# Performance work log

Hardware: AMD Instinct MI355X
Metric: run time of the kernel (lower is better)

Reference implementation:

```python
import jax, jax.numpy as jnp
import numpy as np

LN_EPS = 1e-5


def _ln(x, g, b):
    mu = jnp.mean(x, -1, keepdims=True)
    xc = x - mu
    inv = jax.lax.rsqrt(jnp.mean(xc * xc, -1, keepdims=True) + LN_EPS)
    return xc * inv * g + b


def _subm_conv(x, nbr, W, b):
    # Submanifold 3D conv via rulebook gather-GEMM-accumulate.
    # x: [N, Cin], nbr: [N, K] neighbor row ids (-1 = missing), W: [K, Cin, Cout], b: [Cout]
    N = x.shape[0]
    xp = jnp.concatenate([x, jnp.zeros((1, x.shape[1]), x.dtype)], 0)  # sentinel zero row
    idx = jnp.where(nbr < 0, N, nbr)  # missing neighbors -> zero row
    acc0 = jnp.zeros((N, W.shape[-1]), x.dtype) + b
    def body(acc, xs):
        i, Wk = xs  # i: [N], Wk: [Cin, Cout]
        return acc + xp[i] @ Wk, None
    acc, _ = jax.lax.scan(body, acc0, (idx.T, W))
    return acc


def _blk1(x, W, b, g, be):  # 1x1x1 SubMConv + LN + ReLU
    return jax.nn.relu(_ln(x @ W + b, g, be))


def _blk3(x, nbr, W, b, g, be):  # 3x3x3 SubMConv + LN + ReLU
    return jax.nn.relu(_ln(_subm_conv(x, nbr, W, b), g, be))


def setup_inputs() -> dict:
    rng = np.random.default_rng(0)
    B, D, Npb, K = 2, 160, 131072, 27
    dim, half = 64, 32
    # Build random sparse voxel set and the rulebook (neighbor table) like spconv does.
    lookup = np.full((B, D, D, D), -1, np.int64)
    coords = np.zeros((B * Npb, 3), np.int64)
    for b in range(B):
        lin = np.sort(rng.choice(D * D * D, size=Npb, replace=False))
        z, y, x = np.unravel_index(lin, (D, D, D))
        rows = np.arange(b * Npb, (b + 1) * Npb)
        lookup[b, z, y, x] = rows
        coords[rows] = np.stack([z, y, x], 1)
    bidx = np.repeat(np.arange(B), Npb)
    offs = np.stack(np.meshgrid(np.arange(-1, 2), np.arange(-1, 2), np.arange(-1, 2), indexing="ij"), -1).reshape(K, 3)
    nz = coords[:, None, :] + offs[None]  # [N, K, 3]
    valid = ((nz >= 0) & (nz < D)).all(-1)
    nzc = np.clip(nz, 0, D - 1)
    nbr = lookup[bidx[:, None], nzc[..., 0], nzc[..., 1], nzc[..., 2]]
    nbr = np.where(valid, nbr, -1).astype(np.int32)

    key = jax.random.key(0)
    ks = iter(jax.random.split(key, 16))
    f32 = jnp.float32
    d = {"voxel_features": jax.random.normal(next(ks), (B * Npb, dim), f32),
         "nbr_idx": jnp.asarray(nbr)}
    def lnp(c):
        return jnp.ones((c,), f32), jnp.zeros((c,), f32)
    d["W1"] = 0.05 * jax.random.normal(next(ks), (dim, dim), f32); d["b1"] = jnp.zeros((dim,), f32); d["g1"], d["be1"] = lnp(dim)
    d["W2"] = 0.05 * jax.random.normal(next(ks), (dim, dim), f32); d["b2"] = jnp.zeros((dim,), f32); d["g2"], d["be2"] = lnp(dim)
    d["W3"] = 0.05 * jax.random.normal(next(ks), (K, dim, half), f32); d["b3"] = jnp.zeros((half,), f32); d["g3"], d["be3"] = lnp(half)
    d["W4"] = 0.05 * jax.random.normal(next(ks), (K, half, half), f32); d["b4"] = jnp.zeros((half,), f32); d["g4"], d["be4"] = lnp(half)
    d["W5"] = 0.05 * jax.random.normal(next(ks), (K, half, half), f32); d["b5"] = jnp.zeros((half,), f32); d["g5"], d["be5"] = lnp(half)
    d["W6"] = 0.05 * jax.random.normal(next(ks), (K, half, half), f32); d["b6"] = jnp.zeros((half,), f32); d["g6"], d["be6"] = lnp(half)
    d["W7"] = 0.05 * jax.random.normal(next(ks), (4 * dim, dim), f32); d["b7"] = jnp.zeros((dim,), f32); d["g7"], d["be7"] = lnp(dim)
    return d


def reference(voxel_features, nbr_idx,
              W1, b1, g1, be1, W2, b2, g2, be2,
              W3, b3, g3, be3, W4, b4, g4, be4,
              W5, b5, g5, be5, W6, b6, g6, be6,
              W7, b7, g7, be7):
    x = voxel_features
    f1 = _blk1(x, W1, b1, g1, be1)
    f2 = _blk1(x, W2, b2, g2, be2)
    feats = [f1, f2]
    f2 = _blk3(f2, nbr_idx, W3, b3, g3, be3); feats.append(f2)
    f2 = _blk3(f2, nbr_idx, W4, b4, g4, be4); feats.append(f2)
    f2 = _blk3(f2, nbr_idx, W5, b5, g5, be5); feats.append(f2)
    f2 = _blk3(f2, nbr_idx, W6, b6, g6, be6); feats.append(f2)
    cat = jnp.concatenate(feats, -1)  # [N, 4*dim]
    return _blk1(cat, W7, b7, g7, be7)
```

## Files before the change

kernel.cpp:

```cpp
#include <hip/hip_runtime.h>

typedef __attribute__((ext_vector_type(4))) float  float4_;
typedef __attribute__((ext_vector_type(8))) short  short8;
typedef __attribute__((ext_vector_type(8))) __bf16 bf16x8;

__device__ inline unsigned short f2bf(float f) {
    unsigned u = __builtin_bit_cast(unsigned, f);
    u += 0x7FFFu + ((u >> 16) & 1u);
    return (unsigned short)(u >> 16);
}

__device__ inline float4_ mfma16(bf16x8 a, bf16x8 b, float4_ c) {
    return __builtin_amdgcn_mfma_f32_16x16x32_bf16(a, b, c, 0, 0, 0);
}

__device__ inline void packW_one(const float* __restrict__ src, unsigned short* __restrict__ dst,
                                 int cin, int cout, int e) {
    int f = e >> 9, i = e & 511, lane = i >> 3, t = i & 7;
    int ntn = cout >> 4, ctn = cin >> 5;
    int nt = f % ntn;
    int rest = f / ntn;
    int ct = rest % ctn;
    int k = rest / ctn;
    int c = ct * 32 + (lane >> 4) * 8 + t;
    int j = nt * 16 + (lane & 15);
    dst[e] = f2bf(src[(k * cin + c) * cout + j]);
}

__global__ void pack_all_kernel(
    const float* __restrict__ W1, const float* __restrict__ W2,
    const float* __restrict__ W3, const float* __restrict__ W4,
    const float* __restrict__ W5, const float* __restrict__ W6,
    const float* __restrict__ W7,
    unsigned short* cat, unsigned short* Wp12, unsigned short* Wp3,
    unsigned short* Wp4, unsigned short* Wp5, unsigned short* Wp6,
    unsigned short* Wp7, int N) {
    int e = blockIdx.x * 256 + threadIdx.x;
    if (e < 8192) {
        int f = e >> 9, i = e & 511, lane = i >> 3, t = i & 7;
        int nt = f & 7, ct = f >> 3;
        int c = ct * 32 + (lane >> 4) * 8 + t;
        int j = nt * 16 + (lane & 15);
        float v = (j < 64) ? W1[c * 64 + j] : W2[c * 64 + (j - 64)];
        Wp12[e] = f2bf(v);
        return;
    }
    e -= 8192;
    if (e < 55296) { packW_one(W3, Wp3, 64, 32, e); return; }
    e -= 55296;
    if (e < 27648) { packW_one(W4, Wp4, 32, 32, e); return; }
    e -= 27648;
    if (e < 27648) { packW_one(W5, Wp5, 32, 32, e); return; }
    e -= 27648;
    if (e < 27648) { packW_one(W6, Wp6, 32, 32, e); return; }
    e -= 27648;
    if (e < 16384) { packW_one(W7, Wp7, 256, 64, e); return; }
    e -= 16384;
    if (e < 128) ((unsigned*)(cat + (size_t)N * 256))[e] = 0;
}

__global__ __launch_bounds__(256) void blk12_kernel(
    const float* __restrict__ x, unsigned short* cat,
    const unsigned short* __restrict__ Wp,
    const float* __restrict__ b1, const float* __restrict__ g1, const float* __restrict__ be1,
    const float* __restrict__ b2, const float* __restrict__ g2, const float* __restrict__ be2) {
    int tid = threadIdx.x, lane = tid & 63, wv = tid >> 6;
    int l15 = lane & 15, q = lane >> 4;
    long base = ((long)blockIdx.x * 4 + wv) * 16;

    float4_ acc[8];
#pragma unroll
    for (int i = 0; i < 8; i++) acc[i] = (float4_){0.f, 0.f, 0.f, 0.f};

#pragma unroll
    for (int kt = 0; kt < 2; kt++) {
        const float* xp = x + (base + l15) * 64 + kt * 32 + q * 8;
        float4_ f0 = *(const float4_*)xp;
        float4_ f1 = *(const float4_*)(xp + 4);
        short8 as;
        as[0] = (short)f2bf(f0[0]); as[1] = (short)f2bf(f0[1]);
        as[2] = (short)f2bf(f0[2]); as[3] = (short)f2bf(f0[3]);
        as[4] = (short)f2bf(f1[0]); as[5] = (short)f2bf(f1[1]);
        as[6] = (short)f2bf(f1[2]); as[7] = (short)f2bf(f1[3]);
        bf16x8 a = __builtin_bit_cast(bf16x8, as);
        const unsigned short* wp = Wp + (size_t)kt * 8 * 512;
#pragma unroll
        for (int nt = 0; nt < 8; nt++) {
            bf16x8 w = *(const bf16x8*)(wp + nt * 512 + lane * 8);
            acc[nt] = mfma16(a, w, acc[nt]);
        }
    }

    float bc[8], gc[8], bec[8];
#pragma unroll
    for (int nt = 0; nt < 8; nt++) {
        int j = nt * 16 + l15;
        if (j < 64) { bc[nt] = b1[j]; gc[nt] = g1[j]; bec[nt] = be1[j]; }
        else        { bc[nt] = b2[j - 64]; gc[nt] = g2[j - 64]; bec[nt] = be2[j - 64]; }
    }

#pragma unroll
    for (int r = 0; r < 4; r++) {
        long row = base + q * 4 + r;
        float v[8], s0 = 0.f, s1 = 0.f, q0 = 0.f, q1 = 0.f;
#pragma unroll
        for (int nt = 0; nt < 4; nt++) { v[nt] = acc[nt][r] + bc[nt]; s0 += v[nt]; q0 += v[nt] * v[nt]; }
#pragma unroll
        for (int nt = 4; nt < 8; nt++) { v[nt] = acc[nt][r] + bc[nt]; s1 += v[nt]; q1 += v[nt] * v[nt]; }
#pragma unroll
        for (int m = 1; m < 16; m <<= 1) {
            s0 += __shfl_xor(s0, m); q0 += __shfl_xor(q0, m);
            s1 += __shfl_xor(s1, m); q1 += __shfl_xor(q1, m);
        }
        float mu0 = s0 * (1.f / 64), var0 = q0 * (1.f / 64) - mu0 * mu0, inv0 = rsqrtf(var0 + 1e-5f);
        float mu1 = s1 * (1.f / 64), var1 = q1 * (1.f / 64) - mu1 * mu1, inv1 = rsqrtf(var1 + 1e-5f);
        unsigned short* cp = cat + row * 256;
#pragma unroll
        for (int nt = 0; nt < 4; nt++) {
            float y = fmaxf((v[nt] - mu0) * inv0 * gc[nt] + bec[nt], 0.f);
            cp[nt * 16 + l15] = f2bf(y);
        }
#pragma unroll
        for (int nt = 4; nt < 8; nt++) {
            float y = fmaxf((v[nt] - mu1) * inv1 * gc[nt] + bec[nt], 0.f);
            cp[nt * 16 + l15] = f2bf(y);
        }
    }
}

template <int CT, int D>
__global__ __launch_bounds__(256) void conv_kernel(
    unsigned short* cat, const int* __restrict__ nbr,
    const unsigned short* __restrict__ Wp,
    const float* __restrict__ bb, const float* __restrict__ gg, const float* __restrict__ bee,
    int in_off, int out_off, int N) {
    const int MT = 2;
    int tid = threadIdx.x, lane = tid & 63, wv = tid >> 6;
    int l15 = lane & 15, q = lane >> 4;
    int G = gridDim.x;
    int eff = (blockIdx.x & 7) * (G >> 3) + (blockIdx.x >> 3);
    long base = ((long)eff * 4 + wv) * 32;

    float4_ acc[MT][2];
#pragma unroll
    for (int mt = 0; mt < MT; mt++) {
        acc[mt][0] = (float4_){0.f, 0.f, 0.f, 0.f};
        acc[mt][1] = (float4_){0.f, 0.f, 0.f, 0.f};
    }

    const unsigned short* catp = cat + in_off + q * 8;
    const unsigned short* wl = Wp + lane * 8;
    const int* nbp[MT];
#pragma unroll
    for (int mt = 0; mt < MT; mt++) nbp[mt] = nbr + (base + mt * 16 + l15) * 27;

    bf16x8 f[D + 1][MT][CT];
    bf16x8 wr[3][CT][2];
    int rawi[3][MT];

    int raw0[D + 2][MT];
#pragma unroll
    for (int j = 0; j < D + 2; j++)
#pragma unroll
        for (int mt = 0; mt < MT; mt++) raw0[j][mt] = nbp[mt][j];

#pragma unroll
    for (int kk = 0; kk < 2; kk++)
#pragma unroll
        for (int ct = 0; ct < CT; ct++)
#pragma unroll
            for (int nt = 0; nt < 2; nt++)
                wr[kk][ct][nt] = *(const bf16x8*)(wl + ((size_t)((kk * CT + ct) * 2 + nt)) * 512);

#pragma unroll
    for (int j = 0; j < D; j++)
#pragma unroll
        for (int mt = 0; mt < MT; mt++) {
            int v = raw0[j][mt];
            size_t s = (size_t)(v < 0 ? N : v);
#pragma unroll
            for (int ct = 0; ct < CT; ct++)
                f[j][mt][ct] = *(const bf16x8*)(catp + s * 256 + ct * 32);
        }
#pragma unroll
    for (int mt = 0; mt < MT; mt++) {
        rawi[D % 3][mt] = raw0[D][mt];
        rawi[(D + 1) % 3][mt] = raw0[D + 1][mt];
    }

#pragma unroll
    for (int k = 0; k < 27; k++) {
        if (k + 2 < 27) {
#pragma unroll
            for (int ct = 0; ct < CT; ct++)
#pragma unroll
                for (int nt = 0; nt < 2; nt++)
                    wr[(k + 2) % 3][ct][nt] =
                        *(const bf16x8*)(wl + ((size_t)(((k + 2) * CT + ct) * 2 + nt)) * 512);
        }
        if (k + D < 27) {
#pragma unroll
            for (int mt = 0; mt < MT; mt++) {
                int v = rawi[(k + D) % 3][mt];
                size_t s = (size_t)(v < 0 ? N : v);
#pragma unroll
                for (int ct = 0; ct < CT; ct++)
                    f[(k + D) % (D + 1)][mt][ct] = *(const bf16x8*)(catp + s * 256 + ct * 32);
            }
        }
        if (k + D + 2 < 27) {
#pragma unroll
            for (int mt = 0; mt < MT; mt++) rawi[(k + D + 2) % 3][mt] = nbp[mt][k + D + 2];
        }
#pragma unroll
        for (int ct = 0; ct < CT; ct++) {
            bf16x8 w0 = wr[k % 3][ct][0];
            bf16x8 w1 = wr[k % 3][ct][1];
#pragma unroll
            for (int mt = 0; mt < MT; mt++) {
                acc[mt][0] = mfma16(f[k % (D + 1)][mt][ct], w0, acc[mt][0]);
                acc[mt][1] = mfma16(f[k % (D + 1)][mt][ct], w1, acc[mt][1]);
            }
        }
    }

    float b0c = bb[l15], b1c = bb[16 + l15];
    float g0c = gg[l15], g1c = gg[16 + l15];
    float be0c = bee[l15], be1c = bee[16 + l15];

#pragma unroll
    for (int mt = 0; mt < MT; mt++) {
#pragma unroll
        for (int r = 0; r < 4; r++) {
            long row = base + mt * 16 + q * 4 + r;
            float v0 = acc[mt][0][r] + b0c;
            float v1 = acc[mt][1][r] + b1c;
            float s = v0 + v1, sq = v0 * v0 + v1 * v1;
#pragma unroll
            for (int m = 1; m < 16; m <<= 1) { s += __shfl_xor(s, m); sq += __shfl_xor(sq, m); }
            float mu = s * (1.f / 32), var = sq * (1.f / 32) - mu * mu, inv = rsqrtf(var + 1e-5f);
            float y0 = fmaxf((v0 - mu) * inv * g0c + be0c, 0.f);
            float y1 = fmaxf((v1 - mu) * inv * g1c + be1c, 0.f);
            unsigned short* cp = cat + row * 256 + out_off;
            cp[l15] = f2bf(y0);
            cp[16 + l15] = f2bf(y1);
        }
    }
}

__global__ __launch_bounds__(256) void blk7_kernel(
    const unsigned short* __restrict__ cat, const unsigned short* __restrict__ Wp,
    const float* __restrict__ b, const float* __restrict__ g, const float* __restrict__ be,
    float* __restrict__ out) {
    int tid = threadIdx.x, lane = tid & 63, wv = tid >> 6;
    int l15 = lane & 15, q = lane >> 4;
    long base = ((long)blockIdx.x * 4 + wv) * 16;

    float4_ acc[4];
#pragma unroll
    for (int i = 0; i < 4; i++) acc[i] = (float4_){0.f, 0.f, 0.f, 0.f};

#pragma unroll
    for (int kt = 0; kt < 8; kt++) {
        bf16x8 a = *(const bf16x8*)(cat + (base + l15) * 256 + kt * 32 + q * 8);
        const unsigned short* wp = Wp + (size_t)kt * 4 * 512;
#pragma unroll
        for (int nt = 0; nt < 4; nt++) {
            bf16x8 w = *(const bf16x8*)(wp + nt * 512 + lane * 8);
            acc[nt] = mfma16(a, w, acc[nt]);
        }
    }

    float bc[4], gc[4], bec[4];
#pragma unroll
    for (int nt = 0; nt < 4; nt++) {
        int j = nt * 16 + l15;
        bc[nt] = b[j]; gc[nt] = g[j]; bec[nt] = be[j];
    }

#pragma unroll
    for (int r = 0; r < 4; r++) {
        long row = base + q * 4 + r;
        float v[4], s = 0.f, sq = 0.f;
#pragma unroll
        for (int nt = 0; nt < 4; nt++) { v[nt] = acc[nt][r] + bc[nt]; s += v[nt]; sq += v[nt] * v[nt]; }
#pragma unroll
        for (int m = 1; m < 16; m <<= 1) { s += __shfl_xor(s, m); sq += __shfl_xor(sq, m); }
        float mu = s * (1.f / 64), var = sq * (1.f / 64) - mu * mu, inv = rsqrtf(var + 1e-5f);
#pragma unroll
        for (int nt = 0; nt < 4; nt++) {
            float y = fmaxf((v[nt] - mu) * inv * gc[nt] + bec[nt], 0.f);
            out[row * 64 + nt * 16 + l15] = y;
        }
    }
}

extern "C" void kernel_launch(void* const* d_in, const int* in_sizes, int n_in,
                              void* d_out, int out_size, void* d_ws, size_t ws_size,
                              hipStream_t stream) {
    const int N = in_sizes[0] / 64;

    const float* x   = (const float*)d_in[0];
    const int*   nbr = (const int*)d_in[1];
    const float* W1 = (const float*)d_in[2];
    const float* b1 = (const float*)d_in[3];
    const float* g1 = (const float*)d_in[4];
    const float* be1 = (const float*)d_in[5];
    const float* W2 = (const float*)d_in[6];
    const float* b2 = (const float*)d_in[7];
    const float* g2 = (const float*)d_in[8];
    const float* be2 = (const float*)d_in[9];
    const float* W3 = (const float*)d_in[10];
    const float* b3 = (const float*)d_in[11];
    const float* g3 = (const float*)d_in[12];
    const float* be3 = (const float*)d_in[13];
    const float* W4 = (const float*)d_in[14];
    const float* b4 = (const float*)d_in[15];
    const float* g4 = (const float*)d_in[16];
    const float* be4 = (const float*)d_in[17];
    const float* W5 = (const float*)d_in[18];
    const float* b5 = (const float*)d_in[19];
    const float* g5 = (const float*)d_in[20];
    const float* be5 = (const float*)d_in[21];
    const float* W6 = (const float*)d_in[22];
    const float* b6 = (const float*)d_in[23];
    const float* g6 = (const float*)d_in[24];
    const float* be6 = (const float*)d_in[25];
    const float* W7 = (const float*)d_in[26];
    const float* b7 = (const float*)d_in[27];
    const float* g7 = (const float*)d_in[28];
    const float* be7 = (const float*)d_in[29];

    unsigned short* ws   = (unsigned short*)d_ws;
    unsigned short* cat  = ws;
    unsigned short* Wp12 = cat + (size_t)(N + 1) * 256;
    unsigned short* Wp3  = Wp12 + 8192;
    unsigned short* Wp4  = Wp3 + 55296;
    unsigned short* Wp5  = Wp4 + 27648;
    unsigned short* Wp6  = Wp5 + 27648;
    unsigned short* Wp7  = Wp6 + 27648;

    pack_all_kernel<<<637, 256, 0, stream>>>(W1, W2, W3, W4, W5, W6, W7,
                                             cat, Wp12, Wp3, Wp4, Wp5, Wp6, Wp7, N);

    blk12_kernel<<<N / 64, 256, 0, stream>>>(x, cat, Wp12, b1, g1, be1, b2, g2, be2);
    conv_kernel<2, 3><<<N / 128, 256, 0, stream>>>(cat, nbr, Wp3, b3, g3, be3, 64, 128, N);
    conv_kernel<1, 4><<<N / 128, 256, 0, stream>>>(cat, nbr, Wp4, b4, g4, be4, 128, 160, N);
    conv_kernel<1, 4><<<N / 128, 256, 0, stream>>>(cat, nbr, Wp5, b5, g5, be5, 160, 192, N);
    conv_kernel<1, 4><<<N / 128, 256, 0, stream>>>(cat, nbr, Wp6, b6, g6, be6, 192, 224, N);
    blk7_kernel<<<N / 64, 256, 0, stream>>>(cat, Wp7, b7, g7, be7, (float*)d_out);
}
```

Before: 447.5 us.

## Transpose neighbor table once and deepen conv prefetch pipeline with sched barriers

Adds a kernel that transposes the neighbor table to [27, N] with missing entries already mapped to the sentinel row, so the conv kernels read coalesced indices instead of strided 27-int rows. The conv kernel's software pipeline is restructured: indices are prefetched 2*D steps ahead, weights D steps ahead in a D+1 ring, and sched_barriers separate the load and MFMA phases. The first conv uses prefetch depth 2 instead of 3. The extra transpose kernel adds a launch and a pass over the neighbor table, and the deeper buffers raise register pressure.

```diff
diff --git a/kernel.cpp b/kernel.cpp
--- a/kernel.cpp
+++ b/kernel.cpp
@@ -59,6 +59,16 @@
     if (e < 128) ((unsigned*)(cat + (size_t)N * 256))[e] = 0;
 }
 
+__global__ void nbrT_kernel(const int* __restrict__ nbr, int* __restrict__ nbrT, int N) {
+    int row = blockIdx.x * 256 + threadIdx.x;
+    if (row >= N) return;
+#pragma unroll
+    for (int k = 0; k < 27; k++) {
+        int v = nbr[(size_t)row * 27 + k];
+        nbrT[(size_t)k * N + row] = v < 0 ? N : v;
+    }
+}
+
 __global__ __launch_bounds__(256) void blk12_kernel(
     const float* __restrict__ x, unsigned short* cat,
     const unsigned short* __restrict__ Wp,
@@ -130,7 +140,7 @@
 
 template <int CT, int D>
 __global__ __launch_bounds__(256) void conv_kernel(
-    unsigned short* cat, const int* __restrict__ nbr,
+    unsigned short* cat, const int* __restrict__ nbrT,
     const unsigned short* __restrict__ Wp,
     const float* __restrict__ bb, const float* __restrict__ gg, const float* __restrict__ bee,
     int in_off, int out_off, int N) {
@@ -150,78 +160,71 @@
 
     const unsigned short* catp = cat + in_off + q * 8;
     const unsigned short* wl = Wp + lane * 8;
-    const int* nbp[MT];
-#pragma unroll
-    for (int mt = 0; mt < MT; mt++) nbp[mt] = nbr + (base + mt * 16 + l15) * 27;
-
+    long r0 = base + l15, r1 = base + 16 + l15;
+
+    int    idxr[D + 1][MT];
     bf16x8 f[D + 1][MT][CT];
-    bf16x8 wr[3][CT][2];
-    int rawi[3][MT];
-
-    int raw0[D + 2][MT];
-#pragma unroll
-    for (int j = 0; j < D + 2; j++)
-#pragma unroll
-        for (int mt = 0; mt < MT; mt++) raw0[j][mt] = nbp[mt][j];
-
-#pragma unroll
-    for (int kk = 0; kk < 2; kk++)
+    bf16x8 wr[D + 1][CT][2];
+
+#pragma unroll
+    for (int j = 0; j < D; j++) {
+        idxr[j][0] = nbrT[(size_t)j * N + r0];
+        idxr[j][1] = nbrT[(size_t)j * N + r1];
+    }
+#pragma unroll
+    for (int j = 0; j < D; j++) {
+#pragma unroll
+        for (int mt = 0; mt < MT; mt++) {
+            size_t s = (size_t)idxr[j % (D + 1)][mt];
+#pragma unroll
+            for (int ct = 0; ct < CT; ct++)
+                f[j % (D + 1)][mt][ct] = *(const bf16x8*)(catp + s * 256 + ct * 32);
+        }
 #pragma unroll
         for (int ct = 0; ct < CT; ct++)
 #pragma unroll
             for (int nt = 0; nt < 2; nt++)
-                wr[kk][ct][nt] = *(const bf16x8*)(wl + ((size_t)((kk * CT + ct) * 2 + nt)) * 512);
-
-#pragma unroll
-    for (int j = 0; j < D; j++)
-#pragma unroll
-        for (int mt = 0; mt < MT; mt++) {
-            int v = raw0[j][mt];
-            size_t s = (size_t)(v < 0 ? N : v);
-#pragma unroll
-            for (int ct = 0; ct < CT; ct++)
-                f[j][mt][ct] = *(const bf16x8*)(catp + s * 256 + ct * 32);
-        }
-#pragma unroll
-    for (int mt = 0; mt < MT; mt++) {
-        rawi[D % 3][mt] = raw0[D][mt];
-        rawi[(D + 1) % 3][mt] = raw0[D + 1][mt];
+                wr[j % (D + 1)][ct][nt] =
+                    *(const bf16x8*)(wl + ((size_t)((j * CT + ct) * 2 + nt)) * 512);
+        if (j + D < 27) {
+            idxr[(j + D) % (D + 1)][0] = nbrT[(size_t)(j + D) * N + r0];
+            idxr[(j + D) % (D + 1)][1] = nbrT[(size_t)(j + D) * N + r1];
+        }
     }
 
 #pragma unroll
     for (int k = 0; k < 27; k++) {
-        if (k + 2 < 27) {
-#pragma unroll
-            for (int ct = 0; ct < CT; ct++)
-#pragma unroll
-                for (int nt = 0; nt < 2; nt++)
-                    wr[(k + 2) % 3][ct][nt] =
-                        *(const bf16x8*)(wl + ((size_t)(((k + 2) * CT + ct) * 2 + nt)) * 512);
-        }
         if (k + D < 27) {
 #pragma unroll
             for (int mt = 0; mt < MT; mt++) {
-                int v = rawi[(k + D) % 3][mt];
-                size_t s = (size_t)(v < 0 ? N : v);
+                size_t s = (size_t)idxr[(k + D) % (D + 1)][mt];
 #pragma unroll
                 for (int ct = 0; ct < CT; ct++)
                     f[(k + D) % (D + 1)][mt][ct] = *(const bf16x8*)(catp + s * 256 + ct * 32);
             }
-        }
-        if (k + D + 2 < 27) {
-#pragma unroll
-            for (int mt = 0; mt < MT; mt++) rawi[(k + D + 2) % 3][mt] = nbp[mt][k + D + 2];
-        }
+#pragma unroll
+            for (int ct = 0; ct < CT; ct++)
+#pragma unroll
+                for (int nt = 0; nt < 2; nt++)
+                    wr[(k + D) % (D + 1)][ct][nt] =
+                        *(const bf16x8*)(wl + ((size_t)(((k + D) * CT + ct) * 2 + nt)) * 512);
+        }
+        if (k + 2 * D < 27) {
+            idxr[(k + 2 * D) % (D + 1)][0] = nbrT[(size_t)(k + 2 * D) * N + r0];
+            idxr[(k + 2 * D) % (D + 1)][1] = nbrT[(size_t)(k + 2 * D) * N + r1];
+        }
+        __builtin_amdgcn_sched_barrier(0);
 #pragma unroll
         for (int ct = 0; ct < CT; ct++) {
-            bf16x8 w0 = wr[k % 3][ct][0];
-            bf16x8 w1 = wr[k % 3][ct][1];
+            bf16x8 w0 = wr[k % (D + 1)][ct][0];
+            bf16x8 w1 = wr[k % (D + 1)][ct][1];
 #pragma unroll
             for (int mt = 0; mt < MT; mt++) {
                 acc[mt][0] = mfma16(f[k % (D + 1)][mt][ct], w0, acc[mt][0]);
                 acc[mt][1] = mfma16(f[k % (D + 1)][mt][ct], w1, acc[mt][1]);
             }
         }
+        __builtin_amdgcn_sched_barrier(0);
     }
 
     float b0c = bb[l15], b1c = bb[16 + l15];
@@ -339,14 +342,17 @@
     unsigned short* Wp5  = Wp4 + 27648;
     unsigned short* Wp6  = Wp5 + 27648;
     unsigned short* Wp7  = Wp6 + 27648;
+    int* nbrT = (int*)(Wp7 + 16384);
+    nbrT = (int*)(((size_t)nbrT + 15) & ~(size_t)15);
 
     pack_all_kernel<<<637, 256, 0, stream>>>(W1, W2, W3, W4, W5, W6, W7,
                                              cat, Wp12, Wp3, Wp4, Wp5, Wp6, Wp7, N);
+    nbrT_kernel<<<(N + 255) / 256, 256, 0, stream>>>(nbr, nbrT, N);
 
     blk12_kernel<<<N / 64, 256, 0, stream>>>(x, cat, Wp12, b1, g1, be1, b2, g2, be2);
-    conv_kernel<2, 3><<<N / 128, 256, 0, stream>>>(cat, nbr, Wp3, b3, g3, be3, 64, 128, N);
-    conv_kernel<1, 4><<<N / 128, 256, 0, stream>>>(cat, nbr, Wp4, b4, g4, be4, 128, 160, N);
-    conv_kernel<1, 4><<<N / 128, 256, 0, stream>>>(cat, nbr, Wp5, b5, g5, be5, 160, 192, N);
-    conv_kernel<1, 4><<<N / 128, 256, 0, stream>>>(cat, nbr, Wp6, b6, g6, be6, 192, 224, N);
+    conv_kernel<2, 2><<<N / 128, 256, 0, stream>>>(cat, nbrT, Wp3, b3, g3, be3, 64, 128, N);
+    conv_kernel<1, 4><<<N / 128, 256, 0, stream>>>(cat, nbrT, Wp4, b4, g4, be4, 128, 160, N);
+    conv_kernel<1, 4><<<N / 128, 256, 0, stream>>>(cat, nbrT, Wp5, b5, g5, be5, 160, 192, N);
+    conv_kernel<1, 4><<<N / 128, 256, 0, stream>>>(cat, nbrT, Wp6, b6, g6, be6, 192, 224, N);
     blk7_kernel<<<N / 64, 256, 0, stream>>>(cat, Wp7, b7, g7, be7, (float*)d_out);
 }
```

Result: no change. 452.1 us (+1.0%).
